# Optimization experiments

Hardware: AMD Instinct MI355X
Metric: run time of the kernel (lower is better)

The kernel has to match this reference:

```python
import jax, jax.numpy as jnp
import numpy as np

D_HEAD = 64
KV_HEADS = 8
Q_HEADS = 32
ROPE_BASE = 10000.0


def rope(x):
    # x: (B, S, H, D); pairs are interleaved along last dim, matching torch view(...,D//2,2)
    B, S, H, D = x.shape
    inv_freq = 1.0 / (ROPE_BASE ** (jnp.arange(0, D, 2, dtype=jnp.float32) / D))
    theta = jnp.arange(S, dtype=jnp.float32)[:, None] * inv_freq[None, :]  # (S, D/2)
    cos = jnp.cos(theta)[None, :, None, :]
    sin = jnp.sin(theta)[None, :, None, :]
    xf = x.astype(jnp.float32).reshape(B, S, H, D // 2, 2)
    x1, x2 = xf[..., 0], xf[..., 1]
    out = jnp.stack((x1 * cos - x2 * sin, x1 * sin + x2 * cos), axis=-1)
    return out.reshape(B, S, H, D).astype(x.dtype)


def setup_inputs() -> dict:
    key = jax.random.key(0)
    ks = jax.random.split(key, 5)
    B, S, D = 2, 2048, 2048
    scale = 1.0 / np.sqrt(D)
    return {
        "x": jax.random.normal(ks[0], (B, S, D), dtype=jnp.float32),
        "Wq": jax.random.normal(ks[1], (Q_HEADS * D_HEAD, D), dtype=jnp.float32) * scale,
        "Wk": jax.random.normal(ks[2], (KV_HEADS * D_HEAD, D), dtype=jnp.float32) * scale,
        "Wv": jax.random.normal(ks[3], (KV_HEADS * D_HEAD, D), dtype=jnp.float32) * scale,
        "Wo": jax.random.normal(ks[4], (D, D), dtype=jnp.float32) * scale,
    }


def reference(x, Wq, Wk, Wv, Wo):
    B, S, D = x.shape
    G = Q_HEADS // KV_HEADS  # query heads per kv head

    Q = (x @ Wq.T).reshape(B, S, Q_HEADS, D_HEAD)
    K = (x @ Wk.T).reshape(B, S, KV_HEADS, D_HEAD)
    V = (x @ Wv.T).reshape(B, S, KV_HEADS, D_HEAD)

    Q = rope(Q)
    K = rope(K)

    # (B, KV, G, S, Dh): group g of kv head h corresponds to q head h*G+g,
    # exactly matching repeat_interleave of K/V along head dim.
    Q = Q.transpose(0, 2, 1, 3).reshape(B, KV_HEADS, G, S, D_HEAD)
    K = K.transpose(0, 2, 1, 3)  # (B, KV, S, Dh)
    V = V.transpose(0, 2, 1, 3)

    scores = jnp.einsum("bkgsd,bktd->bkgst", Q, K) / np.sqrt(D_HEAD).astype(np.float32)
    causal_mask = jnp.tril(jnp.ones((S, S), dtype=bool))
    scores = jnp.where(causal_mask, scores, -jnp.inf)
    probs = jax.nn.softmax(scores, axis=-1)
    attn = jnp.einsum("bkgst,bktd->bkgsd", probs, V)

    attn = attn.reshape(B, Q_HEADS, S, D_HEAD).transpose(0, 2, 1, 3).reshape(B, S, D)
    return attn @ Wo.T
```

## Files before the change

### kernel.cpp

```cpp
#include <hip/hip_runtime.h>
#include <stdint.h>

#define S_LEN   2048
#define D_MODEL 2048
#define DKV     512

typedef __attribute__((ext_vector_type(8))) short short8;
typedef __attribute__((ext_vector_type(4))) float f32x4;

__device__ static inline unsigned short f2bf(float f) {
  unsigned u = __builtin_bit_cast(unsigned, f);
  u += 0x7FFFu + ((u >> 16) & 1u);
  return (unsigned short)(u >> 16);
}
__device__ static inline float bf2f(unsigned short h) {
  return __builtin_bit_cast(float, ((unsigned)h) << 16);
}

__device__ static inline void gload_lds16(const void* g, void* lds) {
  __builtin_amdgcn_global_load_lds((const __attribute__((address_space(1))) void*)g,
                                   (__attribute__((address_space(3))) void*)lds,
                                   16, 0, 0);
}

__global__ __launch_bounds__(256) void cvt_all_kernel(
    const float* __restrict__ x, const float* __restrict__ wq, const float* __restrict__ wk,
    const float* __restrict__ wv, const float* __restrict__ wo,
    unsigned short* __restrict__ xb, unsigned short* __restrict__ wqb,
    unsigned short* __restrict__ wkb, unsigned short* __restrict__ wvb,
    unsigned short* __restrict__ wob) {
  int i = blockIdx.x * 256 + threadIdx.x;
  const float* s; unsigned short* d;
  if (i < 1048576)      { s = x;  d = xb;  }
  else if (i < 1572864) { s = wq; d = wqb; i -= 1048576; }
  else if (i < 1703936) { s = wk; d = wkb; i -= 1572864; }
  else if (i < 1835008) { s = wv; d = wvb; i -= 1703936; }
  else                  { s = wo; d = wob; i -= 1835008; }
  const float4 a = ((const float4*)s)[i * 2];
  const float4 b = ((const float4*)s)[i * 2 + 1];
  unsigned short u[8] = {f2bf(a.x), f2bf(a.y), f2bf(a.z), f2bf(a.w),
                         f2bf(b.x), f2bf(b.y), f2bf(b.z), f2bf(b.w)};
  *(uint4*)(d + (size_t)i * 8) = *(const uint4*)u;
}

__device__ static inline void storeC(unsigned short* C, size_t idx, float v) { C[idx] = f2bf(v); }
__device__ static inline void storeC(float* C, size_t idx, float v) { C[idx] = v; }

template <int CMODE, typename CT>
__device__ __forceinline__ void gemm128_body(const unsigned short* A, int lda,
                                             const unsigned short* B, int ldb,
                                             CT* C, int ldc,
                                             int m0, int n0, int Kdim,
                                             unsigned short* As, unsigned short* Bs) {
  const int tid  = threadIdx.x;
  const int lane = tid & 63;
  const int w    = tid >> 6;
  const int wm   = w >> 1, wn = w & 1;
  const int lcol = lane & 15;
  const int lq   = lane >> 4;

  f32x4 acc[4][4] = {};

  for (int k0 = 0; k0 < Kdim; k0 += 32) {
    __syncthreads();
#pragma unroll
    for (int i = 0; i < 2; ++i) {
      const int c  = i * 4 + w;
      const int e  = c * 512 + lane * 8;
      const int rr = e >> 5;
      const int cc = e & 31;
      gload_lds16(A + (size_t)(m0 + rr) * lda + (k0 + cc), As + c * 512);
      gload_lds16(B + (size_t)(n0 + rr) * ldb + (k0 + cc), Bs + c * 512);
    }
    __syncthreads();

    short8 af[4], bfr[4];
#pragma unroll
    for (int mi = 0; mi < 4; ++mi)
      af[mi] = *(const short8*)&As[(wm * 64 + mi * 16 + lcol) * 32 + lq * 8];
#pragma unroll
    for (int ni = 0; ni < 4; ++ni)
      bfr[ni] = *(const short8*)&Bs[(wn * 64 + ni * 16 + lcol) * 32 + lq * 8];
#pragma unroll
    for (int mi = 0; mi < 4; ++mi)
#pragma unroll
      for (int ni = 0; ni < 4; ++ni)
        acc[mi][ni] = __builtin_amdgcn_mfma_f32_16x16x32_bf16(af[mi], bfr[ni], acc[mi][ni], 0, 0, 0);
  }
#pragma unroll
  for (int mi = 0; mi < 4; ++mi)
#pragma unroll
    for (int ni = 0; ni < 4; ++ni)
#pragma unroll
      for (int r = 0; r < 4; ++r) {
        const int row = m0 + wm * 64 + mi * 16 + lq * 4 + r;
        const int col = n0 + wn * 64 + ni * 16 + lcol;
        if constexpr (CMODE == 1) {
          C[((size_t)((row >> 11) * 512 + col)) * 2048 + (row & 2047)] = f2bf(acc[mi][ni][r]);
        } else {
          storeC(C, (size_t)row * ldc + col, acc[mi][ni][r]);
        }
      }
}

__global__ __launch_bounds__(256) void qkv_gemm_kernel(
    const unsigned short* __restrict__ x,
    const unsigned short* __restrict__ Wq, const unsigned short* __restrict__ Wk,
    const unsigned short* __restrict__ Wv,
    unsigned short* __restrict__ Qo, unsigned short* __restrict__ Ko, unsigned short* __restrict__ Vt) {
  __shared__ unsigned short As[128 * 32];
  __shared__ unsigned short Bs[128 * 32];
  const int tn = blockIdx.x;
  const int m0 = blockIdx.y * 128;
  if (tn < 16) {
    gemm128_body<0>(x, D_MODEL, Wq, D_MODEL, Qo, D_MODEL, m0, tn * 128, D_MODEL, As, Bs);
  } else if (tn < 20) {
    gemm128_body<0>(x, D_MODEL, Wk, D_MODEL, Ko, DKV, m0, (tn - 16) * 128, D_MODEL, As, Bs);
  } else {
    gemm128_body<1>(x, D_MODEL, Wv, D_MODEL, Vt, DKV, m0, (tn - 20) * 128, D_MODEL, As, Bs);
  }
}

__global__ __launch_bounds__(256) void oproj_gemm_kernel(
    const unsigned short* __restrict__ A, const unsigned short* __restrict__ Wo,
    float* __restrict__ C) {
  __shared__ unsigned short As[128 * 32];
  __shared__ unsigned short Bs[128 * 32];
  gemm128_body<0>(A, D_MODEL, Wo, D_MODEL, C, D_MODEL,
                  blockIdx.y * 128, blockIdx.x * 128, D_MODEL, As, Bs);
}

__global__ __launch_bounds__(256) void rope_both_kernel(unsigned short* __restrict__ Qb,
                                                        unsigned short* __restrict__ Kb) {
  int idx = blockIdx.x * 256 + threadIdx.x;
  unsigned short* X; int lgHalf; float scale;
  if (idx < 4194304) { X = Qb; lgHalf = 10; scale = 0.125f; }
  else               { X = Kb; lgHalf = 8;  scale = 1.0f; idx -= 4194304; }
  const int half = 1 << lgHalf;
  const int r  = idx >> lgHalf;
  const int cp = idx & (half - 1);
  const int i  = cp & 31;
  const int s  = r & (S_LEN - 1);
  const float inv = exp2f(-13.287712379549449f * (float)(2 * i) * (1.0f / 64.0f));
  const float th  = (float)s * inv;
  const float c = cosf(th), sn = sinf(th);
  unsigned short* p = X + ((size_t)r << (lgHalf + 1)) + 2 * cp;
  const float x0 = bf2f(p[0]), x1 = bf2f(p[1]);
  p[0] = f2bf((x0 * c - x1 * sn) * scale);
  p[1] = f2bf((x0 * sn + x1 * c) * scale);
}

__global__ __launch_bounds__(256, 4) void attn_kernel(const unsigned short* __restrict__ Q,
                                                      const unsigned short* __restrict__ K,
                                                      const unsigned short* __restrict__ Vt,
                                                      unsigned short* __restrict__ O) {
  const int hq = blockIdx.y;
  const int bb = blockIdx.z;
  const int hk = hq >> 2;
  const int tid  = threadIdx.x;
  const int lane = tid & 63;
  const int w    = tid >> 6;
  const int lcol = lane & 15;
  const int lq   = lane >> 4;
  const int trow = tid >> 2;
  const int tq   = (tid & 3) * 16;

  __shared__ unsigned short QPs[64 * 72];
  __shared__ unsigned short Ks[64 * 72];
  __shared__ unsigned short Vts[64 * 72];

  for (int pass = 0; pass < 2; ++pass) {
    const int qt = pass ? (31 - (int)blockIdx.x) : (int)blockIdx.x;
    const int q0 = qt * 64;
    const int ntiles = qt + 1;
    const int qrow = q0 + w * 16 + lcol;

    uint4 kp0, kp1, vp0, vp1;
    {
      const unsigned short* gk = K + ((size_t)(bb * S_LEN + 0 + trow)) * DKV + hk * 64 + tq;
      kp0 = *(const uint4*)gk; kp1 = *(const uint4*)(gk + 8);
      const unsigned short* gv = Vt + ((size_t)(bb * DKV + hk * 64 + trow)) * S_LEN + 0 + tq;
      vp0 = *(const uint4*)gv; vp1 = *(const uint4*)(gv + 8);
    }

    __syncthreads();
    {
      const unsigned short* g = Q + ((size_t)(bb * S_LEN + q0 + trow)) * D_MODEL + hq * 64 + tq;
      *(uint4*)&QPs[trow * 72 + tq]     = *(const uint4*)g;
      *(uint4*)&QPs[trow * 72 + tq + 8] = *(const uint4*)(g + 8);
    }
    __syncthreads();

    short8 qf[2];
#pragma unroll
    for (int ks = 0; ks < 2; ++ks)
      qf[ks] = *(const short8*)&QPs[(w * 16 + lcol) * 72 + ks * 32 + lq * 8];

    f32x4 Oacc[4] = {};
    float m_i = -3e38f, l_i = 0.f;

    for (int it = 0; it < ntiles; ++it) {
      __syncthreads();
      *(uint4*)&Ks[trow * 72 + tq]      = kp0;
      *(uint4*)&Ks[trow * 72 + tq + 8]  = kp1;
      *(uint4*)&Vts[trow * 72 + tq]     = vp0;
      *(uint4*)&Vts[trow * 72 + tq + 8] = vp1;
      if (it + 1 < ntiles) {
        const int t1 = (it + 1) * 64;
        const unsigned short* gk = K + ((size_t)(bb * S_LEN + t1 + trow)) * DKV + hk * 64 + tq;
        kp0 = *(const uint4*)gk; kp1 = *(const uint4*)(gk + 8);
        const unsigned short* gv = Vt + ((size_t)(bb * DKV + hk * 64 + trow)) * S_LEN + t1 + tq;
        vp0 = *(const uint4*)gv; vp1 = *(const uint4*)(gv + 8);
      }
      __syncthreads();

      f32x4 Sacc[4] = {};
#pragma unroll
      for (int ks = 0; ks < 2; ++ks)
#pragma unroll
        for (int nt = 0; nt < 4; ++nt) {
          const short8 kf = *(const short8*)&Ks[(nt * 16 + lcol) * 72 + ks * 32 + lq * 8];
          Sacc[nt] = __builtin_amdgcn_mfma_f32_16x16x32_bf16(kf, qf[ks], Sacc[nt], 0, 0, 0);
        }

      if (it == ntiles - 1) {
#pragma unroll
        for (int nt = 0; nt < 4; ++nt)
#pragma unroll
          for (int r = 0; r < 4; ++r) {
            const int key = q0 + nt * 16 + lq * 4 + r;
            if (key > qrow) Sacc[nt][r] = -1e30f;
          }
      }

      float mx = fmaxf(fmaxf(Sacc[0][0], Sacc[0][1]), fmaxf(Sacc[0][2], Sacc[0][3]));
#pragma unroll
      for (int nt = 1; nt < 4; ++nt)
        mx = fmaxf(mx, fmaxf(fmaxf(Sacc[nt][0], Sacc[nt][1]), fmaxf(Sacc[nt][2], Sacc[nt][3])));
      mx = fmaxf(mx, __shfl_xor(mx, 16));
      mx = fmaxf(mx, __shfl_xor(mx, 32));
      const float mnew  = fmaxf(m_i, mx);
      const float alpha = __expf(m_i - mnew);
      float rs = 0.f;
#pragma unroll
      for (int nt = 0; nt < 4; ++nt)
#pragma unroll
        for (int r = 0; r < 4; ++r) {
          const float p = __expf(Sacc[nt][r] - mnew);
          Sacc[nt][r] = p;
          rs += p;
        }
      rs += __shfl_xor(rs, 16);
      rs += __shfl_xor(rs, 32);
      m_i = mnew;
      l_i = l_i * alpha + rs;
#pragma unroll
      for (int dt = 0; dt < 4; ++dt) Oacc[dt] *= alpha;

      const int prow = w * 16 + lcol;
#pragma unroll
      for (int nt = 0; nt < 4; ++nt) {
        unsigned short u[4] = {f2bf(Sacc[nt][0]), f2bf(Sacc[nt][1]),
                               f2bf(Sacc[nt][2]), f2bf(Sacc[nt][3])};
        *(uint2*)&QPs[prow * 72 + nt * 16 + lq * 4] = *(const uint2*)u;
      }
      asm volatile("s_waitcnt lgkmcnt(0)" ::: "memory");

#pragma unroll
      for (int ks = 0; ks < 2; ++ks) {
        const short8 pf = *(const short8*)&QPs[(w * 16 + lcol) * 72 + ks * 32 + lq * 8];
#pragma unroll
        for (int dt = 0; dt < 4; ++dt) {
          const short8 vf = *(const short8*)&Vts[(dt * 16 + lcol) * 72 + ks * 32 + lq * 8];
          Oacc[dt] = __builtin_amdgcn_mfma_f32_16x16x32_bf16(vf, pf, Oacc[dt], 0, 0, 0);
        }
      }
    }

    const float inv = 1.0f / l_i;
#pragma unroll
    for (int dt = 0; dt < 4; ++dt) {
      unsigned short u[4] = {f2bf(Oacc[dt][0] * inv), f2bf(Oacc[dt][1] * inv),
                             f2bf(Oacc[dt][2] * inv), f2bf(Oacc[dt][3] * inv)};
      *(uint2*)&O[(size_t)(bb * S_LEN + qrow) * D_MODEL + hq * 64 + dt * 16 + lq * 4] =
          *(const uint2*)u;
    }
  }
}

extern "C" void kernel_launch(void* const* d_in, const int* in_sizes, int n_in,
                              void* d_out, int out_size, void* d_ws, size_t ws_size,
                              hipStream_t stream) {
  const float* x  = (const float*)d_in[0];
  const float* Wq = (const float*)d_in[1];
  const float* Wk = (const float*)d_in[2];
  const float* Wv = (const float*)d_in[3];
  const float* Wo = (const float*)d_in[4];
  float* out = (float*)d_out;

  unsigned short* Qb  = (unsigned short*)d_ws;
  unsigned short* Kb  = Qb  + (size_t)4096 * 2048;
  unsigned short* Vtg = Kb  + (size_t)4096 * 512;
  unsigned short* Ab  = Vtg + (size_t)1024 * 2048;
  unsigned short* xb  = Ab  + (size_t)4096 * 2048;
  unsigned short* Wqb = xb  + (size_t)4096 * 2048;
  unsigned short* Wkb = Wqb + (size_t)2048 * 2048;
  unsigned short* Wvb = Wkb + (size_t)512 * 2048;
  unsigned short* Wob = Wvb + (size_t)512 * 2048;

  cvt_all_kernel<<<9216, 256, 0, stream>>>(x, Wq, Wk, Wv, Wo, xb, Wqb, Wkb, Wvb, Wob);

  qkv_gemm_kernel<<<dim3(24, 32), 256, 0, stream>>>(xb, Wqb, Wkb, Wvb, Qb, Kb, Vtg);
  rope_both_kernel<<<20480, 256, 0, stream>>>(Qb, Kb);
  attn_kernel<<<dim3(16, 32, 2), 256, 0, stream>>>(Qb, Kb, Vtg, Ab);
  oproj_gemm_kernel<<<dim3(16, 32), 256, 0, stream>>>(Ab, Wob, out);
}
```

Measured before the change: 323.9 us.

## Process paired causal query tiles together sharing K/V tiles, use exp2 softmax

The attention kernel now handles its two causal-balanced query tiles concurrently instead of in two sequential passes. Each K/V tile is loaded into LDS once and reused for both tiles, which removes the duplicate K/V loads for the shorter tile. Q is prescaled by log2(e)/8 in the RoPE kernel so the softmax can use exp2f. Probabilities are packed to bf16 by truncation with a byte permute instead of round-to-nearest. In exchange the kernel uses more LDS and registers (two accumulator sets), which may lower occupancy, and the truncation slightly reduces precision.

```diff
diff --git a/kernel.cpp b/kernel.cpp
--- a/kernel.cpp
+++ b/kernel.cpp
@@ -15,6 +15,10 @@
 }
 __device__ static inline float bf2f(unsigned short h) {
   return __builtin_bit_cast(float, ((unsigned)h) << 16);
+}
+__device__ static inline unsigned packtrunc2(float f0, float f1) {
+  return __builtin_amdgcn_perm(__builtin_bit_cast(unsigned, f1),
+                               __builtin_bit_cast(unsigned, f0), 0x07060302u);
 }
 
 __device__ static inline void gload_lds16(const void* g, void* lds) {
@@ -134,7 +138,7 @@
                                                         unsigned short* __restrict__ Kb) {
   int idx = blockIdx.x * 256 + threadIdx.x;
   unsigned short* X; int lgHalf; float scale;
-  if (idx < 4194304) { X = Qb; lgHalf = 10; scale = 0.125f; }
+  if (idx < 4194304) { X = Qb; lgHalf = 10; scale = 0.1803368801111244f; }
   else               { X = Kb; lgHalf = 8;  scale = 1.0f; idx -= 4194304; }
   const int half = 1 << lgHalf;
   const int r  = idx >> lgHalf;
@@ -165,126 +169,169 @@
   const int trow = tid >> 2;
   const int tq   = (tid & 3) * 16;
 
-  __shared__ unsigned short QPs[64 * 72];
   __shared__ unsigned short Ks[64 * 72];
   __shared__ unsigned short Vts[64 * 72];
-
-  for (int pass = 0; pass < 2; ++pass) {
-    const int qt = pass ? (31 - (int)blockIdx.x) : (int)blockIdx.x;
-    const int q0 = qt * 64;
-    const int ntiles = qt + 1;
-    const int qrow = q0 + w * 16 + lcol;
-
-    uint4 kp0, kp1, vp0, vp1;
-    {
-      const unsigned short* gk = K + ((size_t)(bb * S_LEN + 0 + trow)) * DKV + hk * 64 + tq;
+  __shared__ unsigned short Pa[64 * 72];
+  __shared__ unsigned short Pb[64 * 72];
+
+  const int qtA = blockIdx.x;
+  const int qtB = 31 - qtA;
+  const int qA0 = qtA * 64, qB0 = qtB * 64;
+  const int qrowA = qA0 + w * 16 + lcol;
+  const int qrowB = qB0 + w * 16 + lcol;
+  const int prow  = w * 16 + lcol;
+
+  uint4 kp0, kp1, vp0, vp1;
+  {
+    const unsigned short* gk = K + ((size_t)(bb * S_LEN + trow)) * DKV + hk * 64 + tq;
+    kp0 = *(const uint4*)gk; kp1 = *(const uint4*)(gk + 8);
+    const unsigned short* gv = Vt + ((size_t)(bb * DKV + hk * 64 + trow)) * S_LEN + tq;
+    vp0 = *(const uint4*)gv; vp1 = *(const uint4*)(gv + 8);
+  }
+
+  {
+    const unsigned short* ga = Q + ((size_t)(bb * S_LEN + qA0 + trow)) * D_MODEL + hq * 64 + tq;
+    *(uint4*)&Pa[trow * 72 + tq]     = *(const uint4*)ga;
+    *(uint4*)&Pa[trow * 72 + tq + 8] = *(const uint4*)(ga + 8);
+    const unsigned short* gb = Q + ((size_t)(bb * S_LEN + qB0 + trow)) * D_MODEL + hq * 64 + tq;
+    *(uint4*)&Pb[trow * 72 + tq]     = *(const uint4*)gb;
+    *(uint4*)&Pb[trow * 72 + tq + 8] = *(const uint4*)(gb + 8);
+  }
+  asm volatile("s_waitcnt lgkmcnt(0)" ::: "memory");
+
+  short8 qfA[2], qfB[2];
+#pragma unroll
+  for (int ks = 0; ks < 2; ++ks) {
+    qfA[ks] = *(const short8*)&Pa[prow * 72 + ks * 32 + lq * 8];
+    qfB[ks] = *(const short8*)&Pb[prow * 72 + ks * 32 + lq * 8];
+  }
+
+  f32x4 OaccA[4] = {}, OaccB[4] = {};
+  float mA = -3e38f, lA = 0.f, mB = -3e38f, lB = 0.f;
+
+  auto softmax_update = [&](f32x4 (&S)[4], float& m_i, float& l_i, f32x4 (&Oacc)[4],
+                            unsigned short* P) {
+    float mx = fmaxf(fmaxf(S[0][0], S[0][1]), fmaxf(S[0][2], S[0][3]));
+#pragma unroll
+    for (int nt = 1; nt < 4; ++nt)
+      mx = fmaxf(mx, fmaxf(fmaxf(S[nt][0], S[nt][1]), fmaxf(S[nt][2], S[nt][3])));
+    mx = fmaxf(mx, __shfl_xor(mx, 16));
+    mx = fmaxf(mx, __shfl_xor(mx, 32));
+    const float mnew  = fmaxf(m_i, mx);
+    const float alpha = exp2f(m_i - mnew);
+    float rs = 0.f;
+#pragma unroll
+    for (int nt = 0; nt < 4; ++nt)
+#pragma unroll
+      for (int r = 0; r < 4; ++r) {
+        const float p = exp2f(S[nt][r] - mnew);
+        S[nt][r] = p;
+        rs += p;
+      }
+    rs += __shfl_xor(rs, 16);
+    rs += __shfl_xor(rs, 32);
+    m_i = mnew;
+    l_i = l_i * alpha + rs;
+#pragma unroll
+    for (int dt = 0; dt < 4; ++dt) Oacc[dt] *= alpha;
+#pragma unroll
+    for (int nt = 0; nt < 4; ++nt) {
+      unsigned u2[2] = {packtrunc2(S[nt][0], S[nt][1]), packtrunc2(S[nt][2], S[nt][3])};
+      *(uint2*)&P[prow * 72 + nt * 16 + lq * 4] = *(const uint2*)u2;
+    }
+  };
+
+  for (int t = 0; t <= qtB; ++t) {
+    __syncthreads();
+    *(uint4*)&Ks[trow * 72 + tq]      = kp0;
+    *(uint4*)&Ks[trow * 72 + tq + 8]  = kp1;
+    *(uint4*)&Vts[trow * 72 + tq]     = vp0;
+    *(uint4*)&Vts[trow * 72 + tq + 8] = vp1;
+    if (t < qtB) {
+      const int t1 = (t + 1) * 64;
+      const unsigned short* gk = K + ((size_t)(bb * S_LEN + t1 + trow)) * DKV + hk * 64 + tq;
       kp0 = *(const uint4*)gk; kp1 = *(const uint4*)(gk + 8);
-      const unsigned short* gv = Vt + ((size_t)(bb * DKV + hk * 64 + trow)) * S_LEN + 0 + tq;
+      const unsigned short* gv = Vt + ((size_t)(bb * DKV + hk * 64 + trow)) * S_LEN + t1 + tq;
       vp0 = *(const uint4*)gv; vp1 = *(const uint4*)(gv + 8);
     }
-
     __syncthreads();
-    {
-      const unsigned short* g = Q + ((size_t)(bb * S_LEN + q0 + trow)) * D_MODEL + hq * 64 + tq;
-      *(uint4*)&QPs[trow * 72 + tq]     = *(const uint4*)g;
-      *(uint4*)&QPs[trow * 72 + tq + 8] = *(const uint4*)(g + 8);
-    }
-    __syncthreads();
-
-    short8 qf[2];
+
+    const bool actA = (t <= qtA);
+
+    f32x4 SB[4] = {};
 #pragma unroll
     for (int ks = 0; ks < 2; ++ks)
-      qf[ks] = *(const short8*)&QPs[(w * 16 + lcol) * 72 + ks * 32 + lq * 8];
-
-    f32x4 Oacc[4] = {};
-    float m_i = -3e38f, l_i = 0.f;
-
-    for (int it = 0; it < ntiles; ++it) {
-      __syncthreads();
-      *(uint4*)&Ks[trow * 72 + tq]      = kp0;
-      *(uint4*)&Ks[trow * 72 + tq + 8]  = kp1;
-      *(uint4*)&Vts[trow * 72 + tq]     = vp0;
-      *(uint4*)&Vts[trow * 72 + tq + 8] = vp1;
-      if (it + 1 < ntiles) {
-        const int t1 = (it + 1) * 64;
-        const unsigned short* gk = K + ((size_t)(bb * S_LEN + t1 + trow)) * DKV + hk * 64 + tq;
-        kp0 = *(const uint4*)gk; kp1 = *(const uint4*)(gk + 8);
-        const unsigned short* gv = Vt + ((size_t)(bb * DKV + hk * 64 + trow)) * S_LEN + t1 + tq;
-        vp0 = *(const uint4*)gv; vp1 = *(const uint4*)(gv + 8);
-      }
-      __syncthreads();
-
-      f32x4 Sacc[4] = {};
+#pragma unroll
+      for (int nt = 0; nt < 4; ++nt) {
+        const short8 kf = *(const short8*)&Ks[(nt * 16 + lcol) * 72 + ks * 32 + lq * 8];
+        SB[nt] = __builtin_amdgcn_mfma_f32_16x16x32_bf16(kf, qfB[ks], SB[nt], 0, 0, 0);
+      }
+    if (t == qtB) {
+#pragma unroll
+      for (int nt = 0; nt < 4; ++nt)
+#pragma unroll
+        for (int r = 0; r < 4; ++r) {
+          const int key = t * 64 + nt * 16 + lq * 4 + r;
+          if (key > qrowB) SB[nt][r] = -1e30f;
+        }
+    }
+    softmax_update(SB, mB, lB, OaccB, Pb);
+
+    if (actA) {
+      f32x4 SA[4] = {};
 #pragma unroll
       for (int ks = 0; ks < 2; ++ks)
 #pragma unroll
         for (int nt = 0; nt < 4; ++nt) {
           const short8 kf = *(const short8*)&Ks[(nt * 16 + lcol) * 72 + ks * 32 + lq * 8];
-          Sacc[nt] = __builtin_amdgcn_mfma_f32_16x16x32_bf16(kf, qf[ks], Sacc[nt], 0, 0, 0);
+          SA[nt] = __builtin_amdgcn_mfma_f32_16x16x32_bf16(kf, qfA[ks], SA[nt], 0, 0, 0);
         }
-
-      if (it == ntiles - 1) {
+      if (t == qtA) {
 #pragma unroll
         for (int nt = 0; nt < 4; ++nt)
 #pragma unroll
           for (int r = 0; r < 4; ++r) {
-            const int key = q0 + nt * 16 + lq * 4 + r;
-            if (key > qrow) Sacc[nt][r] = -1e30f;
+            const int key = t * 64 + nt * 16 + lq * 4 + r;
+            if (key > qrowA) SA[nt][r] = -1e30f;
           }
       }
-
-      float mx = fmaxf(fmaxf(Sacc[0][0], Sacc[0][1]), fmaxf(Sacc[0][2], Sacc[0][3]));
-#pragma unroll
-      for (int nt = 1; nt < 4; ++nt)
-        mx = fmaxf(mx, fmaxf(fmaxf(Sacc[nt][0], Sacc[nt][1]), fmaxf(Sacc[nt][2], Sacc[nt][3])));
-      mx = fmaxf(mx, __shfl_xor(mx, 16));
-      mx = fmaxf(mx, __shfl_xor(mx, 32));
-      const float mnew  = fmaxf(m_i, mx);
-      const float alpha = __expf(m_i - mnew);
-      float rs = 0.f;
-#pragma unroll
-      for (int nt = 0; nt < 4; ++nt)
-#pragma unroll
-        for (int r = 0; r < 4; ++r) {
-          const float p = __expf(Sacc[nt][r] - mnew);
-          Sacc[nt][r] = p;
-          rs += p;
-        }
-      rs += __shfl_xor(rs, 16);
-      rs += __shfl_xor(rs, 32);
-      m_i = mnew;
-      l_i = l_i * alpha + rs;
-#pragma unroll
-      for (int dt = 0; dt < 4; ++dt) Oacc[dt] *= alpha;
-
-      const int prow = w * 16 + lcol;
-#pragma unroll
-      for (int nt = 0; nt < 4; ++nt) {
-        unsigned short u[4] = {f2bf(Sacc[nt][0]), f2bf(Sacc[nt][1]),
-                               f2bf(Sacc[nt][2]), f2bf(Sacc[nt][3])};
-        *(uint2*)&QPs[prow * 72 + nt * 16 + lq * 4] = *(const uint2*)u;
-      }
-      asm volatile("s_waitcnt lgkmcnt(0)" ::: "memory");
-
+      softmax_update(SA, mA, lA, OaccA, Pa);
+    }
+    asm volatile("s_waitcnt lgkmcnt(0)" ::: "memory");
+
+#pragma unroll
+    for (int ks = 0; ks < 2; ++ks) {
+      const short8 pfB = *(const short8*)&Pb[prow * 72 + ks * 32 + lq * 8];
+#pragma unroll
+      for (int dt = 0; dt < 4; ++dt) {
+        const short8 vf = *(const short8*)&Vts[(dt * 16 + lcol) * 72 + ks * 32 + lq * 8];
+        OaccB[dt] = __builtin_amdgcn_mfma_f32_16x16x32_bf16(vf, pfB, OaccB[dt], 0, 0, 0);
+      }
+    }
+    if (actA) {
 #pragma unroll
       for (int ks = 0; ks < 2; ++ks) {
-        const short8 pf = *(const short8*)&QPs[(w * 16 + lcol) * 72 + ks * 32 + lq * 8];
+        const short8 pfA = *(const short8*)&Pa[prow * 72 + ks * 32 + lq * 8];
 #pragma unroll
         for (int dt = 0; dt < 4; ++dt) {
           const short8 vf = *(const short8*)&Vts[(dt * 16 + lcol) * 72 + ks * 32 + lq * 8];
-          Oacc[dt] = __builtin_amdgcn_mfma_f32_16x16x32_bf16(vf, pf, Oacc[dt], 0, 0, 0);
+          OaccA[dt] = __builtin_amdgcn_mfma_f32_16x16x32_bf16(vf, pfA, OaccA[dt], 0, 0, 0);
         }
       }
     }
-
-    const float inv = 1.0f / l_i;
-#pragma unroll
-    for (int dt = 0; dt < 4; ++dt) {
-      unsigned short u[4] = {f2bf(Oacc[dt][0] * inv), f2bf(Oacc[dt][1] * inv),
-                             f2bf(Oacc[dt][2] * inv), f2bf(Oacc[dt][3] * inv)};
-      *(uint2*)&O[(size_t)(bb * S_LEN + qrow) * D_MODEL + hq * 64 + dt * 16 + lq * 4] =
-          *(const uint2*)u;
-    }
+  }
+
+  const float invA = 1.0f / lA, invB = 1.0f / lB;
+#pragma unroll
+  for (int dt = 0; dt < 4; ++dt) {
+    unsigned short ua[4] = {f2bf(OaccA[dt][0] * invA), f2bf(OaccA[dt][1] * invA),
+                            f2bf(OaccA[dt][2] * invA), f2bf(OaccA[dt][3] * invA)};
+    *(uint2*)&O[(size_t)(bb * S_LEN + qrowA) * D_MODEL + hq * 64 + dt * 16 + lq * 4] =
+        *(const uint2*)ua;
+    unsigned short ub[4] = {f2bf(OaccB[dt][0] * invB), f2bf(OaccB[dt][1] * invB),
+                            f2bf(OaccB[dt][2] * invB), f2bf(OaccB[dt][3] * invB)};
+    *(uint2*)&O[(size_t)(bb * S_LEN + qrowB) * D_MODEL + hq * 64 + dt * 16 + lq * 4] =
+        *(const uint2*)ub;
   }
 }
 
```

Result: no change. 323.0 us (-0.3%).
